# Optimization experiments

Hardware: AMD Instinct MI355X
Metric: run time of the kernel (lower is better)

Reference implementation:

```python
import jax, jax.numpy as jnp
import numpy as np

EPS = 1e-5  # torch LayerNorm default


def _layer_norm(x, gamma, beta):
    mu = jnp.mean(x, axis=-1, keepdims=True)
    var = jnp.mean(jnp.square(x - mu), axis=-1, keepdims=True)
    return (x - mu) * jax.lax.rsqrt(var + EPS) * gamma + beta


def setup_inputs() -> dict:
    key = jax.random.key(0)
    ks = jax.random.split(key, 6)
    B, T, S, A, H = 256, 2048, 39, 4, 256
    D = S + A
    observations = jax.random.normal(ks[0], (B, T, S), dtype=jnp.float32)
    actions = jax.random.normal(ks[1], (B, T, A), dtype=jnp.float32)
    # MLP params (orthogonal gain=0.1 in torch; random scale 0.1 here)
    W1 = jax.random.normal(ks[2], (D, H), dtype=jnp.float32) * 0.1
    b1 = jnp.zeros((H,), dtype=jnp.float32)
    g1 = jnp.ones((H,), dtype=jnp.float32)
    beta1 = jnp.zeros((H,), dtype=jnp.float32)
    W2 = jax.random.normal(ks[3], (H, H), dtype=jnp.float32) * 0.1
    b2 = jnp.zeros((H,), dtype=jnp.float32)
    g2 = jnp.ones((H,), dtype=jnp.float32)
    beta2 = jnp.zeros((H,), dtype=jnp.float32)
    W3 = jax.random.normal(ks[4], (H, 1), dtype=jnp.float32) * 0.1
    b3 = jnp.zeros((1,), dtype=jnp.float32)
    return {"observations": observations, "actions": actions,
            "W1": W1, "b1": b1, "g1": g1, "beta1": beta1,
            "W2": W2, "b2": b2, "g2": g2, "beta2": beta2,
            "W3": W3, "b3": b3}


def reference(observations, actions, W1, b1, g1, beta1, W2, b2, g2, beta2, W3, b3):
    # Batched equivalent of the per-(b,t) loop: concat -> (Linear+LN+ReLU) x2 -> Linear(.,1)
    x = jnp.concatenate([observations, actions], axis=-1)  # [B, T, S+A]
    h = jax.nn.relu(_layer_norm(x @ W1 + b1, g1, beta1))    # [B, T, H]
    h = jax.nn.relu(_layer_norm(h @ W2 + b2, g2, beta2))    # [B, T, H]
    r = (h @ W3 + b3)[..., 0]                                # [B, T] per-step reward
    return jnp.sum(r, axis=-1)                               # [B] segment reward
```

## Files before the change

kernel.cpp:

```cpp
#include <hip/hip_runtime.h>
#include <hip/hip_bf16.h>

typedef __attribute__((ext_vector_type(8)))  short short8;
typedef __attribute__((ext_vector_type(4)))  float f32x4;
typedef __attribute__((ext_vector_type(16))) float f32x16;

__device__ __forceinline__ unsigned short f2bf(float x) {
  __hip_bfloat16 h = __float2bfloat16(x);
  return (unsigned short)__builtin_bit_cast(short, h);
}
__device__ __forceinline__ unsigned packbf2(float lo, float hi2) {
  return (unsigned)f2bf(lo) | ((unsigned)f2bf(hi2) << 16);
}
__device__ __forceinline__ short8 pack8(const float* v) {
  union { unsigned u[4]; short8 s; } c;
  #pragma unroll
  for (int j = 0; j < 4; ++j) c.u[j] = packbf2(v[2 * j], v[2 * j + 1]);
  return c.s;
}

__global__ void repack_zero(const float* __restrict__ W1, const float* __restrict__ W2,
                            short* __restrict__ Wp, float* __restrict__ out, int outn) {
  int id = blockIdx.x * 256 + threadIdx.x;
  if (blockIdx.x == 0 && threadIdx.x < outn) out[threadIdx.x] = 0.f;
  if (id >= 152 * 64) return;
  int fragidx = id >> 6, lane = id & 63;
  const float* W; int ks, mt, kmax;
  if (fragidx < 24) { W = W1; ks = fragidx >> 3; mt = fragidx & 7; kmax = 43; }
  else { int f2 = fragidx - 24; W = W2; ks = f2 >> 3; mt = f2 & 7; kmax = 256; }
  int h = 32 * mt + (lane & 31);
  int k0 = 16 * ks + 8 * (lane >> 5);
  short8 v;
  #pragma unroll
  for (int i = 0; i < 8; ++i) {
    int k = k0 + i;
    float x = (k < kmax) ? W[(long)k * 256 + h] : 0.f;
    v[i] = (short)f2bf(x);
  }
  *(short8*)(Wp + (long)fragidx * 512 + lane * 8) = v;
}

#define TILES 8

__launch_bounds__(256, 2)
__global__ void srm3(const float* __restrict__ obs, const float* __restrict__ act,
                     const float* __restrict__ b1, const float* __restrict__ g1,
                     const float* __restrict__ be1,
                     const float* __restrict__ b2, const float* __restrict__ g2,
                     const float* __restrict__ be2,
                     const float* __restrict__ W3, const float* __restrict__ b3,
                     const short* __restrict__ Wp, float* __restrict__ out) {
  __shared__ float pb1[256], pg1[256], pe1[256];
  __shared__ float pb2[256], pg2[256], pe2[256], pw3[256];
  __shared__ float2 sq1[4][32], sq2[4][32];
  __shared__ short H1[32 * 256];

  const int tid = threadIdx.x;
  pb1[tid] = b1[tid]; pg1[tid] = g1[tid]; pe1[tid] = be1[tid];
  pb2[tid] = b2[tid]; pg2[tid] = g2[tid]; pe2[tid] = be2[tid];
  pw3[tid] = W3[tid];
  const float b3v = b3[0];

  const int wave = tid >> 6, lane = tid & 63;
  const int l31 = lane & 31, hi = lane >> 5;
  const int mt0 = 2 * wave;

  const short8* W1v = (const short8*)Wp;
  const short8* W2v = (const short8*)(Wp + 24L * 512);
  short8 w1f[3][2], w2f[16][2];
  #pragma unroll
  for (int ks = 0; ks < 3; ++ks)
    #pragma unroll
    for (int j = 0; j < 2; ++j)
      w1f[ks][j] = W1v[(ks * 8 + mt0 + j) * 64 + lane];
  #pragma unroll
  for (int ks = 0; ks < 16; ++ks)
    #pragma unroll
    for (int j = 0; j < 2; ++j)
      w2f[ks][j] = W2v[(ks * 8 + mt0 + j) * 64 + lane];

  __syncthreads();

  const int blockRow0 = blockIdx.x * (TILES * 32);
  const int bidx = blockRow0 >> 11;
  const int swz = (l31 & 7) << 4;
  float ptot = 0.f;

  #pragma unroll 1
  for (int t = 0; t < TILES; ++t) {
    const long n = blockRow0 + t * 32 + l31;

    const float* orow = obs + n * 39;
    const float* arow = act + n * 4;
    short8 bx[3];
    {
      float v[8];
      #pragma unroll
      for (int i = 0; i < 8; ++i) v[i] = orow[8 * hi + i];
      bx[0] = pack8(v);
      #pragma unroll
      for (int i = 0; i < 8; ++i) v[i] = orow[16 + 8 * hi + i];
      bx[1] = pack8(v);
      #pragma unroll
      for (int i = 0; i < 8; ++i) {
        int k = 32 + 8 * hi + i;
        float tv = 0.f;
        if (k < 39) tv = orow[k]; else if (k < 43) tv = arow[k - 39];
        v[i] = tv;
      }
      bx[2] = pack8(v);
    }

    f32x16 acc[2];
    acc[0] = (f32x16)0.f; acc[1] = (f32x16)0.f;

    #pragma unroll
    for (int ks = 0; ks < 3; ++ks) {
      acc[0] = __builtin_amdgcn_mfma_f32_32x32x16_bf16(w1f[ks][0], bx[ks], acc[0], 0, 0, 0);
      acc[1] = __builtin_amdgcn_mfma_f32_32x32x16_bf16(w1f[ks][1], bx[ks], acc[1], 0, 0, 0);
    }

    float s = 0.f, q = 0.f;
    #pragma unroll
    for (int j = 0; j < 2; ++j)
      #pragma unroll
      for (int qq = 0; qq < 4; ++qq) {
        const f32x4 b4 = *(const f32x4*)&pb1[32 * (mt0 + j) + 8 * qq + 4 * hi];
        #pragma unroll
        for (int e = 0; e < 4; ++e) {
          float tv = acc[j][4 * qq + e] + b4[e];
          acc[j][4 * qq + e] = tv;
          s += tv; q += tv * tv;
        }
      }
    s += __shfl_xor(s, 32); q += __shfl_xor(q, 32);
    if (lane < 32) sq1[wave][l31] = make_float2(s, q);
    __syncthreads();
    {
      float2 a0 = sq1[0][l31], a1 = sq1[1][l31], a2 = sq1[2][l31], a3 = sq1[3][l31];
      s = a0.x + a1.x + a2.x + a3.x;
      q = a0.y + a1.y + a2.y + a3.y;
    }
    float mean = s * (1.f / 256.f);
    float rstd = rsqrtf(q * (1.f / 256.f) - mean * mean + 1e-5f);

    #pragma unroll
    for (int j = 0; j < 2; ++j)
      #pragma unroll
      for (int qq = 0; qq < 4; ++qq) {
        const int h0 = 32 * (mt0 + j) + 8 * qq + 4 * hi;
        const f32x4 g4 = *(const f32x4*)&pg1[h0];
        const f32x4 e4 = *(const f32x4*)&pe1[h0];
        float val[4];
        #pragma unroll
        for (int e = 0; e < 4; ++e) {
          float a = rstd * g4[e];
          float c = e4[e] - mean * a;
          val[e] = fmaxf(acc[j][4 * qq + e] * a + c, 0.f);
        }
        unsigned lo = packbf2(val[0], val[1]);
        unsigned hiw = packbf2(val[2], val[3]);
        int byteoff = ((int)l31 * 512 + 2 * h0) ^ swz;
        *(uint2*)((char*)H1 + byteoff) = make_uint2(lo, hiw);
      }
    __syncthreads();

    acc[0] = (f32x16)0.f; acc[1] = (f32x16)0.f;
    #pragma unroll
    for (int ks = 0; ks < 16; ++ks) {
      int byteoff = ((int)l31 * 512 + 32 * ks + 16 * hi) ^ swz;
      short8 bb = *(const short8*)((const char*)H1 + byteoff);
      acc[0] = __builtin_amdgcn_mfma_f32_32x32x16_bf16(w2f[ks][0], bb, acc[0], 0, 0, 0);
      acc[1] = __builtin_amdgcn_mfma_f32_32x32x16_bf16(w2f[ks][1], bb, acc[1], 0, 0, 0);
    }

    s = 0.f; q = 0.f;
    #pragma unroll
    for (int j = 0; j < 2; ++j)
      #pragma unroll
      for (int qq = 0; qq < 4; ++qq) {
        const f32x4 b4 = *(const f32x4*)&pb2[32 * (mt0 + j) + 8 * qq + 4 * hi];
        #pragma unroll
        for (int e = 0; e < 4; ++e) {
          float tv = acc[j][4 * qq + e] + b4[e];
          acc[j][4 * qq + e] = tv;
          s += tv; q += tv * tv;
        }
      }
    s += __shfl_xor(s, 32); q += __shfl_xor(q, 32);
    if (lane < 32) sq2[wave][l31] = make_float2(s, q);
    __syncthreads();
    {
      float2 a0 = sq2[0][l31], a1 = sq2[1][l31], a2 = sq2[2][l31], a3 = sq2[3][l31];
      s = a0.x + a1.x + a2.x + a3.x;
      q = a0.y + a1.y + a2.y + a3.y;
    }
    float mean2 = s * (1.f / 256.f);
    float rstd2 = rsqrtf(q * (1.f / 256.f) - mean2 * mean2 + 1e-5f);

    float p = 0.f;
    #pragma unroll
    for (int j = 0; j < 2; ++j)
      #pragma unroll
      for (int qq = 0; qq < 4; ++qq) {
        const int h0 = 32 * (mt0 + j) + 8 * qq + 4 * hi;
        const f32x4 g4 = *(const f32x4*)&pg2[h0];
        const f32x4 e4 = *(const f32x4*)&pe2[h0];
        const f32x4 w4 = *(const f32x4*)&pw3[h0];
        #pragma unroll
        for (int e = 0; e < 4; ++e) {
          float a = rstd2 * g4[e];
          float c = e4[e] - mean2 * a;
          float val = fmaxf(acc[j][4 * qq + e] * a + c, 0.f);
          p += val * w4[e];
        }
      }
    ptot += p;
  }

  ptot += __shfl_xor(ptot, 32);
  #pragma unroll
  for (int off = 1; off < 32; off <<= 1) ptot += __shfl_xor(ptot, off);
  if (lane == 0) {
    float add = ptot + (wave == 0 ? (float)(TILES * 32) * b3v : 0.f);
    atomicAdd(&out[bidx], add);
  }
}

extern "C" void kernel_launch(void* const* d_in, const int* in_sizes, int n_in,
                              void* d_out, int out_size, void* d_ws, size_t ws_size,
                              hipStream_t stream) {
  const float* obs = (const float*)d_in[0];
  const float* act = (const float*)d_in[1];
  const float* W1  = (const float*)d_in[2];
  const float* b1  = (const float*)d_in[3];
  const float* g1  = (const float*)d_in[4];
  const float* be1 = (const float*)d_in[5];
  const float* W2  = (const float*)d_in[6];
  const float* b2  = (const float*)d_in[7];
  const float* g2  = (const float*)d_in[8];
  const float* be2 = (const float*)d_in[9];
  const float* W3  = (const float*)d_in[10];
  const float* b3  = (const float*)d_in[11];
  float* out = (float*)d_out;

  short* Wp = (short*)d_ws;

  repack_zero<<<38, 256, 0, stream>>>(W1, W2, Wp, out, out_size);

  const int n_rows = 256 * 2048;
  const int n_blocks = n_rows / (TILES * 32);
  srm3<<<n_blocks, 256, 0, stream>>>(obs, act, b1, g1, be1,
                                     b2, g2, be2, W3, b3, Wp, out);
}
```

Before: 348.5 us.

## Split hidden dim across 8 waves, fold b1 into W1 GEMM, double tiles per block

Blocks grow from 256 to 512 threads, so each of 8 waves owns one 32-column tile of the hidden dimension instead of two. This halves per-wave accumulator and W2 register state, which allows 4 blocks per CU and more latency hiding. The first-layer bias is folded into the W1 fragment as an extra K row paired with a constant-1 input, removing the bias add pass. W1 fragments are now read from global memory on every tile instead of staying in registers, and each block processes 16 tiles, which halves the block count and the number of atomics.

```diff
diff --git a/kernel.cpp b/kernel.cpp
--- a/kernel.cpp
+++ b/kernel.cpp
@@ -19,202 +19,181 @@
   return c.s;
 }
 
-__global__ void repack_zero(const float* __restrict__ W1, const float* __restrict__ W2,
+__global__ void repack_zero(const float* __restrict__ W1, const float* __restrict__ b1,
+                            const float* __restrict__ W2,
                             short* __restrict__ Wp, float* __restrict__ out, int outn) {
   int id = blockIdx.x * 256 + threadIdx.x;
   if (blockIdx.x == 0 && threadIdx.x < outn) out[threadIdx.x] = 0.f;
   if (id >= 152 * 64) return;
   int fragidx = id >> 6, lane = id & 63;
-  const float* W; int ks, mt, kmax;
-  if (fragidx < 24) { W = W1; ks = fragidx >> 3; mt = fragidx & 7; kmax = 43; }
-  else { int f2 = fragidx - 24; W = W2; ks = f2 >> 3; mt = f2 & 7; kmax = 256; }
-  int h = 32 * mt + (lane & 31);
-  int k0 = 16 * ks + 8 * (lane >> 5);
   short8 v;
-  #pragma unroll
-  for (int i = 0; i < 8; ++i) {
-    int k = k0 + i;
-    float x = (k < kmax) ? W[(long)k * 256 + h] : 0.f;
-    v[i] = (short)f2bf(x);
+  if (fragidx < 24) {
+    int ks = fragidx >> 3, mt = fragidx & 7;
+    int h = 32 * mt + (lane & 31);
+    int k0 = 16 * ks + 8 * (lane >> 5);
+    #pragma unroll
+    for (int i = 0; i < 8; ++i) {
+      int k = k0 + i;
+      float x = (k < 43) ? W1[(long)k * 256 + h] : ((k == 43) ? b1[h] : 0.f);
+      v[i] = (short)f2bf(x);
+    }
+  } else {
+    int f2 = fragidx - 24;
+    int ks = f2 >> 3, mt = f2 & 7;
+    int h = 32 * mt + (lane & 31);
+    int k0 = 16 * ks + 8 * (lane >> 5);
+    #pragma unroll
+    for (int i = 0; i < 8; ++i)
+      v[i] = (short)f2bf(W2[(long)(k0 + i) * 256 + h]);
   }
   *(short8*)(Wp + (long)fragidx * 512 + lane * 8) = v;
 }
 
-#define TILES 8
-
-__launch_bounds__(256, 2)
-__global__ void srm3(const float* __restrict__ obs, const float* __restrict__ act,
-                     const float* __restrict__ b1, const float* __restrict__ g1,
-                     const float* __restrict__ be1,
+#define TILES 16
+
+__launch_bounds__(512, 4)
+__global__ void srm4(const float* __restrict__ obs, const float* __restrict__ act,
+                     const float* __restrict__ g1, const float* __restrict__ be1,
                      const float* __restrict__ b2, const float* __restrict__ g2,
                      const float* __restrict__ be2,
                      const float* __restrict__ W3, const float* __restrict__ b3,
                      const short* __restrict__ Wp, float* __restrict__ out) {
-  __shared__ float pb1[256], pg1[256], pe1[256];
+  __shared__ float pg1[256], pe1[256];
   __shared__ float pb2[256], pg2[256], pe2[256], pw3[256];
-  __shared__ float2 sq1[4][32], sq2[4][32];
+  __shared__ float2 sq1[8][32], sq2[8][32];
   __shared__ short H1[32 * 256];
 
   const int tid = threadIdx.x;
-  pb1[tid] = b1[tid]; pg1[tid] = g1[tid]; pe1[tid] = be1[tid];
-  pb2[tid] = b2[tid]; pg2[tid] = g2[tid]; pe2[tid] = be2[tid];
-  pw3[tid] = W3[tid];
+  if (tid < 256) {
+    pg1[tid] = g1[tid]; pe1[tid] = be1[tid];
+    pb2[tid] = b2[tid]; pg2[tid] = g2[tid]; pe2[tid] = be2[tid];
+    pw3[tid] = W3[tid];
+  }
   const float b3v = b3[0];
 
   const int wave = tid >> 6, lane = tid & 63;
   const int l31 = lane & 31, hi = lane >> 5;
-  const int mt0 = 2 * wave;
+  const int mt = wave;
 
   const short8* W1v = (const short8*)Wp;
   const short8* W2v = (const short8*)(Wp + 24L * 512);
-  short8 w1f[3][2], w2f[16][2];
-  #pragma unroll
-  for (int ks = 0; ks < 3; ++ks)
-    #pragma unroll
-    for (int j = 0; j < 2; ++j)
-      w1f[ks][j] = W1v[(ks * 8 + mt0 + j) * 64 + lane];
+
+  short8 w2f[16];
   #pragma unroll
   for (int ks = 0; ks < 16; ++ks)
-    #pragma unroll
-    for (int j = 0; j < 2; ++j)
-      w2f[ks][j] = W2v[(ks * 8 + mt0 + j) * 64 + lane];
+    w2f[ks] = W2v[(ks * 8 + mt) * 64 + lane];
 
   __syncthreads();
 
   const int blockRow0 = blockIdx.x * (TILES * 32);
   const int bidx = blockRow0 >> 11;
-  const int swz = (l31 & 7) << 4;
+  const int swz = (l31 & 15) << 4;
   float ptot = 0.f;
 
   #pragma unroll 1
   for (int t = 0; t < TILES; ++t) {
     const long n = blockRow0 + t * 32 + l31;
-
     const float* orow = obs + n * 39;
     const float* arow = act + n * 4;
-    short8 bx[3];
+
+    f32x16 acc = (f32x16)0.f;
     {
       float v[8];
       #pragma unroll
       for (int i = 0; i < 8; ++i) v[i] = orow[8 * hi + i];
-      bx[0] = pack8(v);
+      short8 bb = pack8(v);
+      acc = __builtin_amdgcn_mfma_f32_32x32x16_bf16(W1v[(0 * 8 + mt) * 64 + lane], bb, acc, 0, 0, 0);
       #pragma unroll
       for (int i = 0; i < 8; ++i) v[i] = orow[16 + 8 * hi + i];
-      bx[1] = pack8(v);
+      bb = pack8(v);
+      acc = __builtin_amdgcn_mfma_f32_32x32x16_bf16(W1v[(1 * 8 + mt) * 64 + lane], bb, acc, 0, 0, 0);
       #pragma unroll
       for (int i = 0; i < 8; ++i) {
         int k = 32 + 8 * hi + i;
-        float tv = 0.f;
-        if (k < 39) tv = orow[k]; else if (k < 43) tv = arow[k - 39];
+        float tv;
+        if (k < 39) tv = orow[k];
+        else if (k < 43) tv = arow[k - 39];
+        else tv = (k == 43) ? 1.f : 0.f;
         v[i] = tv;
       }
-      bx[2] = pack8(v);
-    }
-
-    f32x16 acc[2];
-    acc[0] = (f32x16)0.f; acc[1] = (f32x16)0.f;
-
-    #pragma unroll
-    for (int ks = 0; ks < 3; ++ks) {
-      acc[0] = __builtin_amdgcn_mfma_f32_32x32x16_bf16(w1f[ks][0], bx[ks], acc[0], 0, 0, 0);
-      acc[1] = __builtin_amdgcn_mfma_f32_32x32x16_bf16(w1f[ks][1], bx[ks], acc[1], 0, 0, 0);
+      bb = pack8(v);
+      acc = __builtin_amdgcn_mfma_f32_32x32x16_bf16(W1v[(2 * 8 + mt) * 64 + lane], bb, acc, 0, 0, 0);
     }
 
     float s = 0.f, q = 0.f;
     #pragma unroll
-    for (int j = 0; j < 2; ++j)
-      #pragma unroll
-      for (int qq = 0; qq < 4; ++qq) {
-        const f32x4 b4 = *(const f32x4*)&pb1[32 * (mt0 + j) + 8 * qq + 4 * hi];
-        #pragma unroll
-        for (int e = 0; e < 4; ++e) {
-          float tv = acc[j][4 * qq + e] + b4[e];
-          acc[j][4 * qq + e] = tv;
-          s += tv; q += tv * tv;
-        }
-      }
+    for (int r = 0; r < 16; ++r) { float z = acc[r]; s += z; q += z * z; }
     s += __shfl_xor(s, 32); q += __shfl_xor(q, 32);
     if (lane < 32) sq1[wave][l31] = make_float2(s, q);
     __syncthreads();
-    {
-      float2 a0 = sq1[0][l31], a1 = sq1[1][l31], a2 = sq1[2][l31], a3 = sq1[3][l31];
-      s = a0.x + a1.x + a2.x + a3.x;
-      q = a0.y + a1.y + a2.y + a3.y;
-    }
+    s = 0.f; q = 0.f;
+    #pragma unroll
+    for (int j = 0; j < 8; ++j) { float2 a2 = sq1[j][l31]; s += a2.x; q += a2.y; }
     float mean = s * (1.f / 256.f);
     float rstd = rsqrtf(q * (1.f / 256.f) - mean * mean + 1e-5f);
 
     #pragma unroll
-    for (int j = 0; j < 2; ++j)
-      #pragma unroll
-      for (int qq = 0; qq < 4; ++qq) {
-        const int h0 = 32 * (mt0 + j) + 8 * qq + 4 * hi;
-        const f32x4 g4 = *(const f32x4*)&pg1[h0];
-        const f32x4 e4 = *(const f32x4*)&pe1[h0];
-        float val[4];
-        #pragma unroll
-        for (int e = 0; e < 4; ++e) {
-          float a = rstd * g4[e];
-          float c = e4[e] - mean * a;
-          val[e] = fmaxf(acc[j][4 * qq + e] * a + c, 0.f);
-        }
-        unsigned lo = packbf2(val[0], val[1]);
-        unsigned hiw = packbf2(val[2], val[3]);
-        int byteoff = ((int)l31 * 512 + 2 * h0) ^ swz;
-        *(uint2*)((char*)H1 + byteoff) = make_uint2(lo, hiw);
-      }
+    for (int qq = 0; qq < 4; ++qq) {
+      const int h0 = 32 * mt + 8 * qq + 4 * hi;
+      const f32x4 g4 = *(const f32x4*)&pg1[h0];
+      const f32x4 e4 = *(const f32x4*)&pe1[h0];
+      float val[4];
+      #pragma unroll
+      for (int e = 0; e < 4; ++e) {
+        float a = rstd * g4[e];
+        float c = fmaf(-mean, a, e4[e]);
+        val[e] = fmaxf(fmaf(acc[4 * qq + e], a, c), 0.f);
+      }
+      unsigned lo = packbf2(val[0], val[1]);
+      unsigned hw = packbf2(val[2], val[3]);
+      int byteoff = (l31 * 512 + 2 * h0) ^ swz;
+      *(uint2*)((char*)H1 + byteoff) = make_uint2(lo, hw);
+    }
     __syncthreads();
 
-    acc[0] = (f32x16)0.f; acc[1] = (f32x16)0.f;
+    acc = (f32x16)0.f;
     #pragma unroll
     for (int ks = 0; ks < 16; ++ks) {
-      int byteoff = ((int)l31 * 512 + 32 * ks + 16 * hi) ^ swz;
+      int byteoff = (l31 * 512 + 32 * ks + 16 * hi) ^ swz;
       short8 bb = *(const short8*)((const char*)H1 + byteoff);
-      acc[0] = __builtin_amdgcn_mfma_f32_32x32x16_bf16(w2f[ks][0], bb, acc[0], 0, 0, 0);
-      acc[1] = __builtin_amdgcn_mfma_f32_32x32x16_bf16(w2f[ks][1], bb, acc[1], 0, 0, 0);
+      acc = __builtin_amdgcn_mfma_f32_32x32x16_bf16(w2f[ks], bb, acc, 0, 0, 0);
     }
 
     s = 0.f; q = 0.f;
     #pragma unroll
-    for (int j = 0; j < 2; ++j)
-      #pragma unroll
-      for (int qq = 0; qq < 4; ++qq) {
-        const f32x4 b4 = *(const f32x4*)&pb2[32 * (mt0 + j) + 8 * qq + 4 * hi];
-        #pragma unroll
-        for (int e = 0; e < 4; ++e) {
-          float tv = acc[j][4 * qq + e] + b4[e];
-          acc[j][4 * qq + e] = tv;
-          s += tv; q += tv * tv;
-        }
-      }
+    for (int qq = 0; qq < 4; ++qq) {
+      const f32x4 b4 = *(const f32x4*)&pb2[32 * mt + 8 * qq + 4 * hi];
+      #pragma unroll
+      for (int e = 0; e < 4; ++e) {
+        float z = acc[4 * qq + e] + b4[e];
+        acc[4 * qq + e] = z;
+        s += z; q += z * z;
+      }
+    }
     s += __shfl_xor(s, 32); q += __shfl_xor(q, 32);
     if (lane < 32) sq2[wave][l31] = make_float2(s, q);
     __syncthreads();
-    {
-      float2 a0 = sq2[0][l31], a1 = sq2[1][l31], a2 = sq2[2][l31], a3 = sq2[3][l31];
-      s = a0.x + a1.x + a2.x + a3.x;
-      q = a0.y + a1.y + a2.y + a3.y;
-    }
+    s = 0.f; q = 0.f;
+    #pragma unroll
+    for (int j = 0; j < 8; ++j) { float2 a2 = sq2[j][l31]; s += a2.x; q += a2.y; }
     float mean2 = s * (1.f / 256.f);
     float rstd2 = rsqrtf(q * (1.f / 256.f) - mean2 * mean2 + 1e-5f);
 
     float p = 0.f;
     #pragma unroll
-    for (int j = 0; j < 2; ++j)
-      #pragma unroll
-      for (int qq = 0; qq < 4; ++qq) {
-        const int h0 = 32 * (mt0 + j) + 8 * qq + 4 * hi;
-        const f32x4 g4 = *(const f32x4*)&pg2[h0];
-        const f32x4 e4 = *(const f32x4*)&pe2[h0];
-        const f32x4 w4 = *(const f32x4*)&pw3[h0];
-        #pragma unroll
-        for (int e = 0; e < 4; ++e) {
-          float a = rstd2 * g4[e];
-          float c = e4[e] - mean2 * a;
-          float val = fmaxf(acc[j][4 * qq + e] * a + c, 0.f);
-          p += val * w4[e];
-        }
-      }
+    for (int qq = 0; qq < 4; ++qq) {
+      const int h0 = 32 * mt + 8 * qq + 4 * hi;
+      const f32x4 g4 = *(const f32x4*)&pg2[h0];
+      const f32x4 e4 = *(const f32x4*)&pe2[h0];
+      const f32x4 w4 = *(const f32x4*)&pw3[h0];
+      #pragma unroll
+      for (int e = 0; e < 4; ++e) {
+        float a = rstd2 * g4[e];
+        float c = fmaf(-mean2, a, e4[e]);
+        float val = fmaxf(fmaf(acc[4 * qq + e], a, c), 0.f);
+        p = fmaf(val, w4[e], p);
+      }
+    }
     ptot += p;
   }
 
@@ -246,10 +225,10 @@
 
   short* Wp = (short*)d_ws;
 
-  repack_zero<<<38, 256, 0, stream>>>(W1, W2, Wp, out, out_size);
+  repack_zero<<<38, 256, 0, stream>>>(W1, b1, W2, Wp, out, out_size);
 
   const int n_rows = 256 * 2048;
   const int n_blocks = n_rows / (TILES * 32);
-  srm3<<<n_blocks, 256, 0, stream>>>(obs, act, b1, g1, be1,
+  srm4<<<n_blocks, 512, 0, stream>>>(obs, act, g1, be1,
                                      b2, g2, be2, W3, b3, Wp, out);
 }
```

After: 460.1 us. 1.32x slower.
